# Kernel optimization log

Measured on AMD Instinct MI355X. Metric: run time of the kernel, lower is better.

The kernel has to match this reference:

```python
import jax, jax.numpy as jnp
import numpy as np

N = 50000
IN_F = 128
OUT_F = 128
NRELA = 128
E1 = 400000
E2 = 100000
ALPHA = 0.2   # LeakyReLU slope
D = 0.85      # PageRank damping
EPS = 1e-12


def setup_inputs() -> dict:
    key = jax.random.key(0)
    ks = jax.random.split(key, 8)
    return {
        "input": jax.random.normal(ks[0], (N, IN_F), dtype=jnp.float32),
        "edge": jax.random.randint(ks[1], (2, E1), 0, N, dtype=jnp.int64),
        "edge_embed": jax.random.normal(ks[2], (E1, NRELA), dtype=jnp.float32),
        "edge_list_nhop": jax.random.randint(ks[3], (2, E2), 0, N, dtype=jnp.int64),
        "edge_embed_nhop": jax.random.normal(ks[4], (E2, NRELA), dtype=jnp.float32),
        "entity_rank": jax.random.uniform(ks[5], (N,), dtype=jnp.float32),
        "a": 0.05 * jax.random.normal(ks[6], (OUT_F, 2 * IN_F + NRELA), dtype=jnp.float32),
        "a_2": 0.05 * jax.random.normal(ks[7], (1, OUT_F), dtype=jnp.float32),
    }


def reference(input, edge, edge_embed, edge_list_nhop, edge_embed_nhop, entity_rank, a, a_2):
    n = input.shape[0]
    # concat n-hop edges (len(edge_list_nhop) != 0 path in the original)
    e = jnp.concatenate([edge, edge_list_nhop], axis=1)          # [2, E]
    emb = jnp.concatenate([edge_embed, edge_embed_nhop], axis=0) # [E, nrela]
    src, dst = e[0], e[1]

    # edge MLP: edge_h = [x_src | x_dst | rel]  -> a @ edge_h^T, leakyrelu
    edge_h = jnp.concatenate([input[src], input[dst], emb], axis=1)   # [E, 2*in+nrela]
    edge_m = jax.nn.leaky_relu(edge_h @ a.T, ALPHA)                   # [E, out]
    powers = -jax.nn.leaky_relu(edge_m @ a_2[0], ALPHA)               # [E]
    edge_e = jnp.exp(powers)                                          # [E]

    # softmax-like normalization over incoming edges of each target node
    a_rowsum = jax.ops.segment_sum(edge_e, dst, num_segments=n)       # [N]
    a_rowsum = jnp.where(a_rowsum == 0.0, EPS, a_rowsum)
    rel_att = edge_e / a_rowsum[dst]                                  # [E]

    # PageRank-style rank update
    e_rowsum = jax.ops.segment_sum(rel_att, src, num_segments=n)      # [N] (out-sum)
    e_rowsum = jnp.where(e_rowsum == 0.0, EPS, e_rowsum)
    val = rel_att * entity_rank[src] / e_rowsum[src]                  # [E]
    e_colsum = jax.ops.segment_sum(val, dst, num_segments=n)          # [N]
    new_rank = 1.0 - D + D * e_colsum                                 # [N]

    # rank-weighted attention propagation of edge features
    edge_prop = (rel_att * new_rank[src])[:, None] * edge_m           # [E, out]
    h_prime = jax.ops.segment_sum(edge_prop, dst, num_segments=n)     # [N, out]

    return jax.nn.elu(h_prime), new_rank
```

## Files before the change

kernel.cpp:

```cpp
#include <hip/hip_runtime.h>
#include <math.h>

#define N_NODES 50000
#define E1N 400000
#define E2N 100000
#define E_TOT 500000
#define ALPHAC 0.2f
#define DAMP 0.85f
#define EPSC 1e-12f

typedef __bf16 bf16_t;
typedef __bf16 bf16x4 __attribute__((ext_vector_type(4)));
typedef __bf16 bf16x8 __attribute__((ext_vector_type(8)));
typedef _Float16 f16_t;
typedef _Float16 f16x4 __attribute__((ext_vector_type(4)));
typedef float f32x4 __attribute__((ext_vector_type(4)));
typedef float f32x16 __attribute__((ext_vector_type(16)));

__device__ __forceinline__ float lrelu(float x) { return x > 0.f ? x : ALPHAC * x; }

__global__ __launch_bounds__(256) void k_pack12(const float* __restrict__ a,
                                                bf16_t* __restrict__ bp) {
  int i = blockIdx.x * 256 + threadIdx.x;
  if (i >= 32768) return;
  int j = i & 7;
  int l = (i >> 3) & 63;
  int nt = (i >> 9) & 7;
  int ks = i >> 12;
  int c = nt * 32 + (l & 31);
  int o = (c < 128) ? c : c - 128;
  int koff = (c < 128) ? 0 : 128;
  int k = ks * 16 + ((l >> 5) << 3) + j;
  bp[i] = (bf16_t)a[o * 384 + koff + k];
}

__global__ __launch_bounds__(256) void k_pack3(const float* __restrict__ a,
                                               bf16_t* __restrict__ bp) {
  int i = blockIdx.x * 256 + threadIdx.x;
  if (i >= 16384) return;
  int j = i & 7;
  int l = (i >> 3) & 63;
  int nt = (i >> 9) & 3;
  int ks = i >> 11;
  int o = nt * 32 + (l & 31);
  int k = ks * 16 + ((l >> 5) << 3) + j;
  bp[i] = (bf16_t)a[o * 384 + 256 + k];
}

__global__ __launch_bounds__(256) void k_pack3c(const float* __restrict__ a,
                                                bf16_t* __restrict__ bp) {
  int i = blockIdx.x * 256 + threadIdx.x;
  if (i >= 16384) return;
  int j = i & 7;
  int l = (i >> 3) & 63;
  int nt = (i >> 9) & 7;
  int ks = i >> 12;
  int o = nt * 16 + (l & 15);
  int k = ks * 32 + ((l >> 4) << 3) + j;
  bp[i] = (bf16_t)a[o * 384 + 256 + k];
}

__global__ __launch_bounds__(256) void k_cnt(const int* __restrict__ edge,
                                             const int* __restrict__ nhop,
                                             int stride, int* __restrict__ cnt) {
  int e = blockIdx.x * 256 + threadIdx.x;
  if (e >= E_TOT) return;
  int d = (e < E1N) ? edge[(size_t)(E1N + e) * stride]
                    : nhop[(size_t)(E2N + (e - E1N)) * stride];
  atomicAdd(&cnt[d], 1);
}

__global__ __launch_bounds__(256) void k_edges(const int* __restrict__ edge,
                                               const int* __restrict__ nhop,
                                               int* __restrict__ sidx,
                                               int* __restrict__ didx, int stride) {
  int e = blockIdx.x * 256 + threadIdx.x;
  if (e >= E_TOT) return;
  int s, d;
  if (e < E1N) {
    s = edge[(size_t)e * stride];
    d = edge[(size_t)(E1N + e) * stride];
  } else {
    int t = e - E1N;
    s = nhop[(size_t)t * stride];
    d = nhop[(size_t)(E2N + t) * stride];
  }
  sidx[e] = s;
  didx[e] = d;
}

__global__ __launch_bounds__(256) void k_scan(const int* __restrict__ cnt,
                                              int* __restrict__ csr_start,
                                              int* __restrict__ cursor) {
  __shared__ int ls[256];
  __shared__ int lofs[256];
  int t = threadIdx.x;
  int lo = t * 196, hi = lo + 196;
  if (hi > N_NODES) hi = N_NODES;
  int s = 0;
  for (int i = lo; i < hi; ++i) s += cnt[i];
  ls[t] = s;
  __syncthreads();
  if (t == 0) {
    int run = 0;
    for (int i = 0; i < 256; ++i) { lofs[i] = run; run += ls[i]; }
  }
  __syncthreads();
  int run = lofs[t];
  for (int i = lo; i < hi; ++i) {
    csr_start[i] = run;
    cursor[i] = run;
    run += cnt[i];
  }
}

__global__ __launch_bounds__(256) void k_pos2(const int* __restrict__ edge,
                                              const int* __restrict__ nhop,
                                              int stride, int* __restrict__ cursor,
                                              int* __restrict__ epos,
                                              int* __restrict__ sidx_s,
                                              int* __restrict__ didx_s) {
  int e = blockIdx.x * 256 + threadIdx.x;
  if (e >= E_TOT) return;
  int s, d;
  if (e < E1N) {
    s = edge[(size_t)e * stride];
    d = edge[(size_t)(E1N + e) * stride];
  } else {
    int t = e - E1N;
    s = nhop[(size_t)t * stride];
    d = nhop[(size_t)(E2N + t) * stride];
  }
  int pos = atomicAdd(&cursor[d], 1);
  epos[e] = pos;
  sidx_s[pos] = s;
  didx_s[pos] = d;
}

__global__ __launch_bounds__(256) void k_uv2(const float* __restrict__ input,
                                             const bf16_t* __restrict__ bp12,
                                             bf16_t* __restrict__ uv) {
  const int tid = threadIdx.x, lane = tid & 63, wv = tid >> 6;
  const int blk = blockIdx.x >> 1, half = blockIdx.x & 1;
  const int ntoff = half * 4;
  const int n0 = blk * 128 + wv * 32;
  const int m = lane & 31, hi2 = lane >> 5;
  int n = n0 + m;
  if (n >= N_NODES) n = 0;
  const float* ar = input + (size_t)n * 128 + hi2 * 8;
  const bf16x8* bp = (const bf16x8*)bp12;

  f32x16 acc[4];
#pragma unroll
  for (int nt = 0; nt < 4; ++nt)
#pragma unroll
    for (int r = 0; r < 16; ++r) acc[nt][r] = 0.f;

#pragma unroll
  for (int ks = 0; ks < 8; ++ks) {
    float4 u0 = *(const float4*)(ar + ks * 16);
    float4 u1 = *(const float4*)(ar + ks * 16 + 4);
    bf16x8 af = {(bf16_t)u0.x, (bf16_t)u0.y, (bf16_t)u0.z, (bf16_t)u0.w,
                 (bf16_t)u1.x, (bf16_t)u1.y, (bf16_t)u1.z, (bf16_t)u1.w};
#pragma unroll
    for (int nt = 0; nt < 4; ++nt)
      acc[nt] = __builtin_amdgcn_mfma_f32_32x32x16_bf16(
          af, bp[(ks * 8 + ntoff + nt) * 64 + lane], acc[nt], 0, 0, 0);
  }
#pragma unroll
  for (int nt = 0; nt < 4; ++nt)
#pragma unroll
    for (int r = 0; r < 16; ++r) {
      int row = (r & 3) + ((r >> 2) << 3) + (hi2 << 2);
      int node = n0 + row;
      if (node < N_NODES)
        uv[(size_t)node * 256 + (ntoff + nt) * 32 + m] = (bf16_t)acc[nt][r];
    }
}

__global__ __launch_bounds__(256) void k_passA4(
    const float* __restrict__ eemb, const float* __restrict__ eembn,
    const bf16_t* __restrict__ uv, const int* __restrict__ edge,
    const int* __restrict__ nhop, int stride, const int* __restrict__ epos,
    const bf16_t* __restrict__ bp3c, const float* __restrict__ a2,
    float* __restrict__ edge_e_s, float* __restrict__ a_rowsum,
    bf16_t* __restrict__ P) {
  __shared__ __align__(16) char sA[16384];
  __shared__ __align__(16) char sB[32768];
  const int tid = threadIdx.x;
  const long long e0 = (long long)blockIdx.x * 64;
  const int lane = tid & 63;

  const int strow = tid >> 5;
  const int stcol = (tid & 31) * 4;
  float4 rg[8];
#pragma unroll
  for (int s = 0; s < 8; ++s) {
    int row = s * 8 + strow;
    long long e = e0 + row;
    rg[s] = make_float4(0.f, 0.f, 0.f, 0.f);
    if (e < E_TOT) {
      const float* src = (e < E1N) ? eemb + (size_t)e * 128
                                   : eembn + (size_t)(e - E1N) * 128;
      rg[s] = *(const float4*)(src + stcol);
    }
  }
  int4 rb[8];
  {
    const int4* bsrc = (const int4*)bp3c;
#pragma unroll
    for (int i = 0; i < 8; ++i) rb[i] = bsrc[i * 256 + tid];
  }
  const int g = tid >> 5;
  const int ml = tid & 31;
  int sarr[8], darr[8], parr[8];
#pragma unroll
  for (int i = 0; i < 8; ++i) {
    long long e = e0 + i * 8 + g;
    sarr[i] = 0; darr[i] = 0; parr[i] = 0;
    if (e < E_TOT) {
      if (e < E1N) {
        sarr[i] = edge[(size_t)e * stride];
        darr[i] = edge[(size_t)(E1N + e) * stride];
      } else {
        long long t = e - E1N;
        sarr[i] = nhop[(size_t)t * stride];
        darr[i] = nhop[(size_t)(E2N + t) * stride];
      }
      parr[i] = epos[e];
    }
  }
#pragma unroll
  for (int s = 0; s < 8; ++s) {
    int row = s * 8 + strow;
    bf16x4 b = {(bf16_t)rg[s].x, (bf16_t)rg[s].y, (bf16_t)rg[s].z, (bf16_t)rg[s].w};
    *(bf16x4*)(sA + row * 256 + ((stcol * 2) ^ ((row & 7) << 4))) = b;
  }
  {
    int4* bdst = (int4*)sB;
#pragma unroll
    for (int i = 0; i < 8; ++i) bdst[i * 256 + tid] = rb[i];
  }
  const int cl = ml * 4;
  bf16x4 uu[8], vv[8];
#pragma unroll
  for (int i = 0; i < 8; ++i) {
    uu[i] = *(const bf16x4*)(uv + (size_t)sarr[i] * 256 + cl);
    vv[i] = *(const bf16x4*)(uv + (size_t)darr[i] * 256 + 128 + cl);
  }
  __syncthreads();

  const int wv = tid >> 6;
  const int cc = lane & 15, kg = lane >> 4;
  const int arow = wv * 16 + cc;
  const int swz = (arow & 7) << 4;
  const bf16x8* sBv = (const bf16x8*)sB;

  f32x4 acc[8];
#pragma unroll
  for (int nt = 0; nt < 8; ++nt) acc[nt] = (f32x4){0.f, 0.f, 0.f, 0.f};

#pragma unroll
  for (int ks = 0; ks < 4; ++ks) {
    bf16x8 af = *(const bf16x8*)(sA + arow * 256 + ((ks * 64 + kg * 16) ^ swz));
#pragma unroll
    for (int nt = 0; nt < 8; ++nt)
      acc[nt] = __builtin_amdgcn_mfma_f32_16x16x32_bf16(
          af, sBv[(ks * 8 + nt) * 64 + lane], acc[nt], 0, 0, 0);
  }
  __syncthreads();

#pragma unroll
  for (int nt = 0; nt < 8; ++nt)
#pragma unroll
    for (int r = 0; r < 4; ++r) {
      int row = wv * 16 + kg * 4 + r;
      int cb = (nt * 16 + cc) * 2;
      *(f16_t*)(sA + row * 256 + (cb ^ ((row & 7) << 4))) = (f16_t)acc[nt][r];
    }
  __syncthreads();

  {
    const float4 a2v = *(const float4*)(a2 + cl);
#pragma unroll
    for (int i = 0; i < 8; ++i) {
      int row = i * 8 + g;
      long long e = e0 + row;
      if (e < E_TOT) {
        f16x4 cc4 = *(const f16x4*)(sA + row * 256 + ((cl * 2) ^ ((row & 7) << 4)));
        float p0 = lrelu((float)cc4[0] + (float)uu[i][0] + (float)vv[i][0]);
        float p1 = lrelu((float)cc4[1] + (float)uu[i][1] + (float)vv[i][1]);
        float p2 = lrelu((float)cc4[2] + (float)uu[i][2] + (float)vv[i][2]);
        float p3 = lrelu((float)cc4[3] + (float)uu[i][3] + (float)vv[i][3]);
        bf16x4 po = {(bf16_t)p0, (bf16_t)p1, (bf16_t)p2, (bf16_t)p3};
        *(bf16x4*)(P + (size_t)parr[i] * 128 + cl) = po;
        float sac = p0 * a2v.x + p1 * a2v.y + p2 * a2v.z + p3 * a2v.w;
#pragma unroll
        for (int off = 1; off < 32; off <<= 1) sac += __shfl_xor(sac, off, 64);
        if (ml == 0) {
          float ev = expf(-lrelu(sac));
          edge_e_s[parr[i]] = ev;
          atomicAdd(&a_rowsum[darr[i]], ev);
        }
      }
    }
  }
}

__global__ __launch_bounds__(256) void k_hprime_s(
    const bf16_t* __restrict__ P, const int* __restrict__ csr_start,
    const int* __restrict__ cnt, const float* __restrict__ rel_att_s,
    const int* __restrict__ sidx_s, const float* __restrict__ new_rank,
    float* __restrict__ out) {
  int gnode = (blockIdx.x << 3) | (threadIdx.x >> 5);
  if (gnode >= N_NODES) return;
  int m = threadIdx.x & 31;
  int start = csr_start[gnode], deg = cnt[gnode];
  float a0 = 0.f, a1 = 0.f, a2v = 0.f, a3v = 0.f;
  if (deg > 0) {
    float rel_c = rel_att_s[start];
    float rk_c = new_rank[sidx_s[start]];
    bf16x4 p_c = *(const bf16x4*)(P + (size_t)start * 128 + m * 4);
    for (int i = 0; i < deg; ++i) {
      int qn = start + ((i + 1 < deg) ? i + 1 : i);
      float rel_n = rel_att_s[qn];
      float rk_n = new_rank[sidx_s[qn]];
      bf16x4 p_n = *(const bf16x4*)(P + (size_t)qn * 128 + m * 4);
      float we = rel_c * rk_c;
      a0 += we * (float)p_c[0];
      a1 += we * (float)p_c[1];
      a2v += we * (float)p_c[2];
      a3v += we * (float)p_c[3];
      rel_c = rel_n; rk_c = rk_n; p_c = p_n;
    }
  }
  float4 r;
  r.x = a0 > 0.f ? a0 : expm1f(a0);
  r.y = a1 > 0.f ? a1 : expm1f(a1);
  r.z = a2v > 0.f ? a2v : expm1f(a2v);
  r.w = a3v > 0.f ? a3v : expm1f(a3v);
  *(float4*)(out + (size_t)gnode * 128 + m * 4) = r;
}

template <bool ACCUM>
__global__ __launch_bounds__(256, 3) void k_pass(
    const float* __restrict__ eemb, const float* __restrict__ eembn,
    const bf16_t* __restrict__ uv, const int* __restrict__ sidx,
    const int* __restrict__ didx, const bf16_t* __restrict__ bp3,
    const float* __restrict__ a2, float* __restrict__ edge_e,
    float* __restrict__ a_rowsum, const float* __restrict__ rel_att,
    const float* __restrict__ new_rank, float* __restrict__ hout) {
  __shared__ bf16_t s_sum[128][136];
  const int tid = threadIdx.x;
  const long long e0 = (long long)blockIdx.x * 128;
  {
    const int g = tid >> 5;
    const int cl = (tid & 31) * 4;
#pragma unroll
    for (int i = 0; i < 16; ++i) {
      int el = i * 8 + g;
      long long e = e0 + el;
      float sx = 0.f, sy = 0.f, sz = 0.f, sw = 0.f;
      if (e < E_TOT) {
        int s = sidx[e], d = didx[e];
        bf16x4 u = *(const bf16x4*)(uv + (size_t)s * 256 + cl);
        bf16x4 v = *(const bf16x4*)(uv + (size_t)d * 256 + 128 + cl);
        sx = (float)u[0] + (float)v[0];
        sy = (float)u[1] + (float)v[1];
        sz = (float)u[2] + (float)v[2];
        sw = (float)u[3] + (float)v[3];
      }
      bf16x4 o = {(bf16_t)sx, (bf16_t)sy, (bf16_t)sz, (bf16_t)sw};
      *(bf16x4*)&s_sum[el][cl] = o;
    }
  }
  __syncthreads();

  const int lane = tid & 63;
  const int wv = tid >> 6;
  const long long e0w = e0 + wv * 32;
  if (e0w >= E_TOT) return;
  const int m = lane & 31, hi2 = lane >> 5;
  const long long e = e0w + m;
  const float* b2 = (e < E1N) ? (eemb + (size_t)e * 128)
                              : (eembn + (size_t)(e - E1N) * 128);
  const float* ar = b2 + hi2 * 8;

  const bf16x8* bp = (const bf16x8*)bp3;
  f32x16 acc[4];
#pragma unroll
  for (int nt = 0; nt < 4; ++nt)
#pragma unroll
    for (int r = 0; r < 16; ++r) acc[nt][r] = 0.f;

  auto loadA = [&](int ks) -> bf16x8 {
    float4 u0 = *(const float4*)(ar + ks * 16);
    float4 u1 = *(const float4*)(ar + ks * 16 + 4);
    bf16x8 rr = {(bf16_t)u0.x, (bf16_t)u0.y, (bf16_t)u0.z, (bf16_t)u0.w,
                 (bf16_t)u1.x, (bf16_t)u1.y, (bf16_t)u1.z, (bf16_t)u1.w};
    return rr;
  };

  bf16x8 a_cur = loadA(0);
  bf16x8 bb[4], bn[4];
#pragma unroll
  for (int nt = 0; nt < 4; ++nt) bb[nt] = bp[nt * 64 + lane];

#pragma unroll
  for (int ks = 0; ks < 8; ++ks) {
    bf16x8 a_nxt;
    if (ks < 7) {
      a_nxt = loadA(ks + 1);
#pragma unroll
      for (int nt = 0; nt < 4; ++nt) bn[nt] = bp[((ks + 1) * 4 + nt) * 64 + lane];
    }
#pragma unroll
    for (int nt = 0; nt < 4; ++nt)
      acc[nt] = __builtin_amdgcn_mfma_f32_32x32x16_bf16(a_cur, bb[nt], acc[nt], 0, 0, 0);
    a_cur = a_nxt;
#pragma unroll
    for (int nt = 0; nt < 4; ++nt) bb[nt] = bn[nt];
  }

  if (!ACCUM) {
    float sac[16];
#pragma unroll
    for (int r = 0; r < 16; ++r) sac[r] = 0.f;
#pragma unroll
    for (int nt = 0; nt < 4; ++nt) {
      float a2v = a2[nt * 32 + m];
      int o = nt * 32 + m;
#pragma unroll
      for (int r = 0; r < 16; ++r) {
        int row = (r & 3) + ((r >> 2) << 3) + (hi2 << 2);
        float c = acc[nt][r] + (float)s_sum[wv * 32 + row][o];
        sac[r] += lrelu(c) * a2v;
      }
    }
#pragma unroll
    for (int off = 1; off < 32; off <<= 1) {
#pragma unroll
      for (int r = 0; r < 16; ++r) sac[r] += __shfl_xor(sac[r], off, 64);
    }
    if (m == 0) {
#pragma unroll
      for (int r = 0; r < 16; ++r) {
        int row = (r & 3) + ((r >> 2) << 3) + (hi2 << 2);
        long long ee_i = e0w + row;
        float ev = expf(-lrelu(sac[r]));
        edge_e[ee_i] = ev;
        atomicAdd(&a_rowsum[didx[ee_i]], ev);
      }
    }
  } else {
    float w_m = rel_att[e] * new_rank[sidx[e]];
    int d = didx[e];
    float wr[16];
    int dr[16];
#pragma unroll
    for (int r = 0; r < 16; ++r) {
      int row = (r & 3) + ((r >> 2) << 3) + (hi2 << 2);
      wr[r] = __shfl(w_m, row, 64);
      dr[r] = __shfl(d, row, 64);
    }
#pragma unroll
    for (int nt = 0; nt < 4; ++nt) {
      int o = nt * 32 + m;
#pragma unroll
      for (int r = 0; r < 16; ++r) {
        int row = (r & 3) + ((r >> 2) << 3) + (hi2 << 2);
        float c = acc[nt][r] + (float)s_sum[wv * 32 + row][o];
        atomicAdd(&hout[(size_t)dr[r] * 128 + o], lrelu(c) * wr[r]);
      }
    }
  }
}

__global__ __launch_bounds__(256) void k_relatt(const float* __restrict__ edge_e,
                                                const int* __restrict__ didx,
                                                const int* __restrict__ sidx,
                                                const float* __restrict__ a_rowsum,
                                                float* __restrict__ rel_att,
                                                float* __restrict__ e_rowsum) {
  int e = blockIdx.x * 256 + threadIdx.x;
  if (e >= E_TOT) return;
  float rs = a_rowsum[didx[e]];
  rs = (rs == 0.f) ? EPSC : rs;
  float r = edge_e[e] / rs;
  rel_att[e] = r;
  atomicAdd(&e_rowsum[sidx[e]], r);
}

__global__ __launch_bounds__(256) void k_val(const float* __restrict__ rel_att,
                                             const int* __restrict__ sidx,
                                             const int* __restrict__ didx,
                                             const float* __restrict__ rank,
                                             const float* __restrict__ e_rowsum,
                                             float* __restrict__ e_colsum) {
  int e = blockIdx.x * 256 + threadIdx.x;
  if (e >= E_TOT) return;
  int s = sidx[e];
  float er = e_rowsum[s];
  er = (er == 0.f) ? EPSC : er;
  float val = rel_att[e] * rank[s] / er;
  atomicAdd(&e_colsum[didx[e]], val);
}

__global__ __launch_bounds__(256) void k_rank(const float* __restrict__ e_colsum,
                                              float* __restrict__ new_rank,
                                              float* __restrict__ out_tail) {
  int n = blockIdx.x * 256 + threadIdx.x;
  if (n >= N_NODES) return;
  float nr = 1.f - DAMP + DAMP * e_colsum[n];
  new_rank[n] = nr;
  out_tail[n] = nr;
}

__global__ __launch_bounds__(256) void k_elu(float* __restrict__ h) {
  int i = blockIdx.x * 256 + threadIdx.x;
  if (i < N_NODES * 128) {
    float x = h[i];
    h[i] = x > 0.f ? x : expm1f(x);
  }
}

extern "C" void kernel_launch(void* const* d_in, const int* in_sizes, int n_in,
                              void* d_out, int out_size, void* d_ws, size_t ws_size,
                              hipStream_t stream) {
  const float* input = (const float*)d_in[0];
  const int* edge = (const int*)d_in[1];
  const float* eemb = (const float*)d_in[2];
  const int* enh = (const int*)d_in[3];
  const float* eembn = (const float*)d_in[4];
  const float* rank = (const float*)d_in[5];
  const float* a = (const float*)d_in[6];
  const float* a2 = (const float*)d_in[7];
  float* out = (float*)d_out;

  int estride = (in_sizes[1] == 2 * E1N) ? 1 : 2;

  char* ws = (char*)d_ws;
  bf16_t* bp12 = (bf16_t*)(ws);
  bf16_t* bp3s = (bf16_t*)(ws + 65536);
  bf16_t* uv = (bf16_t*)(ws + 98304);
  int* epos = (int*)(ws + 25698304);
  int* sidx_s = (int*)(ws + 27698304);
  int* didx_s = (int*)(ws + 29698304);
  float* edge_e_s = (float*)(ws + 31698304);
  int* csr_start = (int*)(ws + 33698304);
  int* cursor = (int*)(ws + 33898304);
  int* cnt = (int*)(ws + 34098304);
  float* a_rowsum = (float*)(ws + 34298304);
  float* e_rowsum = (float*)(ws + 34498304);
  float* e_colsum = (float*)(ws + 34698304);
  float* new_rank = (float*)(ws + 34898304);
  bf16_t* P = (bf16_t*)(ws + 35098624);

  const bool big = ws_size >= 163098624ULL;

  const int NB = (E_TOT + 127) / 128;
  const int NB4 = (E_TOT + 63) / 64;
  const int EB = (E_TOT + 255) / 256;
  const int UVB = 2 * ((N_NODES + 127) / 128);

  if (big) {
    hipMemsetAsync(cnt, 0, 4 * 200000, stream);

    k_pack12<<<128, 256, 0, stream>>>(a, bp12);
    k_pack3c<<<64, 256, 0, stream>>>(a, bp3s);
    k_cnt<<<EB, 256, 0, stream>>>(edge, enh, estride, cnt);
    k_scan<<<1, 256, 0, stream>>>(cnt, csr_start, cursor);
    k_pos2<<<EB, 256, 0, stream>>>(edge, enh, estride, cursor, epos, sidx_s, didx_s);
    k_uv2<<<UVB, 256, 0, stream>>>(input, bp12, uv);

    k_passA4<<<NB4, 256, 0, stream>>>(eemb, eembn, uv, edge, enh, estride, epos,
                                      bp3s, a2, edge_e_s, a_rowsum, P);
    k_relatt<<<EB, 256, 0, stream>>>(edge_e_s, didx_s, sidx_s, a_rowsum,
                                     edge_e_s, e_rowsum);
    k_val<<<EB, 256, 0, stream>>>(edge_e_s, sidx_s, didx_s, rank, e_rowsum, e_colsum);
    k_rank<<<(N_NODES + 255) / 256, 256, 0, stream>>>(e_colsum, new_rank,
                                                      out + (size_t)N_NODES * 128);
    k_hprime_s<<<(N_NODES + 7) / 8, 256, 0, stream>>>(P, csr_start, cnt, edge_e_s,
                                                      sidx_s, new_rank, out);
  } else {
    int* sidx_fb = epos;
    int* didx_fb = sidx_s;
    float* rel_fb = (float*)didx_s;
    float* ee_fb = edge_e_s;

    hipMemsetAsync(cnt, 0, 4 * 200000, stream);
    hipMemsetAsync(out, 0, (size_t)N_NODES * 128 * 4, stream);

    k_pack12<<<128, 256, 0, stream>>>(a, bp12);
    k_pack3<<<64, 256, 0, stream>>>(a, bp3s);
    k_edges<<<EB, 256, 0, stream>>>(edge, enh, sidx_fb, didx_fb, estride);
    k_uv2<<<UVB, 256, 0, stream>>>(input, bp12, uv);

    k_pass<false><<<NB, 256, 0, stream>>>(eemb, eembn, uv, sidx_fb, didx_fb, bp3s,
                                          a2, ee_fb, a_rowsum, nullptr, nullptr,
                                          nullptr);
    k_relatt<<<EB, 256, 0, stream>>>(ee_fb, didx_fb, sidx_fb, a_rowsum, rel_fb,
                                     e_rowsum);
    k_val<<<EB, 256, 0, stream>>>(rel_fb, sidx_fb, didx_fb, rank, e_rowsum, e_colsum);
    k_rank<<<(N_NODES + 255) / 256, 256, 0, stream>>>(e_colsum, new_rank,
                                                      out + (size_t)N_NODES * 128);
    k_pass<true><<<NB, 256, 0, stream>>>(eemb, eembn, uv, sidx_fb, didx_fb, bp3s,
                                         a2, nullptr, nullptr, rel_fb, new_rank, out);
    k_elu<<<(N_NODES * 128 + 255) / 256, 256, 0, stream>>>(out);
  }
}
```

Baseline: 753.4 us.

## Rewrite node projection with 16x16 MFMA tiles and read edge-pass weights from global

```diff
diff --git a/kernel.cpp b/kernel.cpp
--- a/kernel.cpp
+++ b/kernel.cpp
@@ -31,6 +31,21 @@
   int o = (c < 128) ? c : c - 128;
   int koff = (c < 128) ? 0 : 128;
   int k = ks * 16 + ((l >> 5) << 3) + j;
+  bp[i] = (bf16_t)a[o * 384 + koff + k];
+}
+
+__global__ __launch_bounds__(256) void k_pack12c(const float* __restrict__ a,
+                                                 bf16_t* __restrict__ bp) {
+  int i = blockIdx.x * 256 + threadIdx.x;
+  if (i >= 32768) return;
+  int j = i & 7;
+  int l = (i >> 3) & 63;
+  int nt = (i >> 9) & 15;
+  int ks = i >> 13;
+  int c = nt * 16 + (l & 15);
+  int o = (c < 128) ? c : c - 128;
+  int koff = (c < 128) ? 0 : 128;
+  int k = ks * 32 + ((l >> 4) << 3) + j;
   bp[i] = (bf16_t)a[o * 384 + koff + k];
 }
 
@@ -178,7 +193,72 @@
     }
 }
 
-__global__ __launch_bounds__(256) void k_passA4(
+__global__ __launch_bounds__(256) void k_uv3(const float* __restrict__ input,
+                                             const bf16_t* __restrict__ bp12c,
+                                             bf16_t* __restrict__ uv) {
+  __shared__ __align__(16) char sA[16384];
+  const int tid = threadIdx.x;
+  const int n0 = blockIdx.x * 64;
+
+#pragma unroll
+  for (int s = 0; s < 8; ++s) {
+    int idx = s * 1024 + tid * 4;
+    int row = idx >> 7, col = idx & 127;
+    int n = n0 + row;
+    float4 u = make_float4(0.f, 0.f, 0.f, 0.f);
+    if (n < N_NODES) u = *(const float4*)(input + (size_t)n * 128 + col);
+    bf16x4 b = {(bf16_t)u.x, (bf16_t)u.y, (bf16_t)u.z, (bf16_t)u.w};
+    *(bf16x4*)(sA + row * 256 + ((col * 2) ^ ((row & 7) << 4))) = b;
+  }
+  __syncthreads();
+
+  const int lane = tid & 63, wv = tid >> 6;
+  const int cc = lane & 15, kg = lane >> 4;
+  const int arow = wv * 16 + cc;
+  const int swz = (arow & 7) << 4;
+  const bf16x8* bp = (const bf16x8*)bp12c;
+
+  f32x4 acc[16];
+#pragma unroll
+  for (int nt = 0; nt < 16; ++nt) acc[nt] = (f32x4){0.f, 0.f, 0.f, 0.f};
+
+#pragma unroll
+  for (int ks = 0; ks < 4; ++ks) {
+    bf16x8 af = *(const bf16x8*)(sA + arow * 256 + ((ks * 64 + kg * 16) ^ swz));
+#pragma unroll
+    for (int nt = 0; nt < 16; ++nt)
+      acc[nt] = __builtin_amdgcn_mfma_f32_16x16x32_bf16(
+          af, bp[(ks * 16 + nt) * 64 + lane], acc[nt], 0, 0, 0);
+  }
+
+#pragma unroll
+  for (int h = 0; h < 2; ++h) {
+    __syncthreads();
+#pragma unroll
+    for (int nt = 0; nt < 8; ++nt)
+#pragma unroll
+      for (int r = 0; r < 4; ++r) {
+        int row = wv * 16 + kg * 4 + r;
+        int cb = (nt * 16 + cc) * 2;
+        *(bf16_t*)(sA + row * 256 + (cb ^ ((row & 7) << 4))) =
+            (bf16_t)acc[h * 8 + nt][r];
+      }
+    __syncthreads();
+    const int rr = tid >> 4;
+    const int cb2 = (tid & 15) * 16;
+#pragma unroll
+    for (int i = 0; i < 4; ++i) {
+      int row = i * 16 + rr;
+      int n = n0 + row;
+      if (n < N_NODES) {
+        bf16x8 v = *(const bf16x8*)(sA + row * 256 + (cb2 ^ ((row & 7) << 4)));
+        *(bf16x8*)(uv + (size_t)n * 256 + h * 128 + (cb2 >> 1)) = v;
+      }
+    }
+  }
+}
+
+__global__ __launch_bounds__(256) void k_passA5(
     const float* __restrict__ eemb, const float* __restrict__ eembn,
     const bf16_t* __restrict__ uv, const int* __restrict__ edge,
     const int* __restrict__ nhop, int stride, const int* __restrict__ epos,
@@ -186,33 +266,27 @@
     float* __restrict__ edge_e_s, float* __restrict__ a_rowsum,
     bf16_t* __restrict__ P) {
   __shared__ __align__(16) char sA[16384];
-  __shared__ __align__(16) char sB[32768];
   const int tid = threadIdx.x;
   const long long e0 = (long long)blockIdx.x * 64;
-  const int lane = tid & 63;
-
-  const int strow = tid >> 5;
-  const int stcol = (tid & 31) * 4;
-  float4 rg[8];
+
 #pragma unroll
   for (int s = 0; s < 8; ++s) {
-    int row = s * 8 + strow;
+    int idx = s * 1024 + tid * 4;
+    int row = idx >> 7, col = idx & 127;
     long long e = e0 + row;
-    rg[s] = make_float4(0.f, 0.f, 0.f, 0.f);
+    float4 u = make_float4(0.f, 0.f, 0.f, 0.f);
     if (e < E_TOT) {
       const float* src = (e < E1N) ? eemb + (size_t)e * 128
                                    : eembn + (size_t)(e - E1N) * 128;
-      rg[s] = *(const float4*)(src + stcol);
-    }
-  }
-  int4 rb[8];
-  {
-    const int4* bsrc = (const int4*)bp3c;
-#pragma unroll
-    for (int i = 0; i < 8; ++i) rb[i] = bsrc[i * 256 + tid];
-  }
+      u = *(const float4*)(src + col);
+    }
+    bf16x4 b = {(bf16_t)u.x, (bf16_t)u.y, (bf16_t)u.z, (bf16_t)u.w};
+    *(bf16x4*)(sA + row * 256 + ((col * 2) ^ ((row & 7) << 4))) = b;
+  }
+
   const int g = tid >> 5;
   const int ml = tid & 31;
+  const int cl = ml * 4;
   int sarr[8], darr[8], parr[8];
 #pragma unroll
   for (int i = 0; i < 8; ++i) {
@@ -230,31 +304,20 @@
       parr[i] = epos[e];
     }
   }
-#pragma unroll
-  for (int s = 0; s < 8; ++s) {
-    int row = s * 8 + strow;
-    bf16x4 b = {(bf16_t)rg[s].x, (bf16_t)rg[s].y, (bf16_t)rg[s].z, (bf16_t)rg[s].w};
-    *(bf16x4*)(sA + row * 256 + ((stcol * 2) ^ ((row & 7) << 4))) = b;
-  }
-  {
-    int4* bdst = (int4*)sB;
-#pragma unroll
-    for (int i = 0; i < 8; ++i) bdst[i * 256 + tid] = rb[i];
-  }
-  const int cl = ml * 4;
+  __syncthreads();
+
   bf16x4 uu[8], vv[8];
 #pragma unroll
   for (int i = 0; i < 8; ++i) {
     uu[i] = *(const bf16x4*)(uv + (size_t)sarr[i] * 256 + cl);
     vv[i] = *(const bf16x4*)(uv + (size_t)darr[i] * 256 + 128 + cl);
   }
-  __syncthreads();
-
-  const int wv = tid >> 6;
+
+  const int lane = tid & 63, wv = tid >> 6;
   const int cc = lane & 15, kg = lane >> 4;
   const int arow = wv * 16 + cc;
   const int swz = (arow & 7) << 4;
-  const bf16x8* sBv = (const bf16x8*)sB;
+  const bf16x8* bp = (const bf16x8*)bp3c;
 
   f32x4 acc[8];
 #pragma unroll
@@ -266,7 +329,7 @@
 #pragma unroll
     for (int nt = 0; nt < 8; ++nt)
       acc[nt] = __builtin_amdgcn_mfma_f32_16x16x32_bf16(
-          af, sBv[(ks * 8 + nt) * 64 + lane], acc[nt], 0, 0, 0);
+          af, bp[(ks * 8 + nt) * 64 + lane], acc[nt], 0, 0, 0);
   }
   __syncthreads();
 
@@ -559,21 +622,22 @@
   const bool big = ws_size >= 163098624ULL;
 
   const int NB = (E_TOT + 127) / 128;
-  const int NB4 = (E_TOT + 63) / 64;
+  const int NB5 = (E_TOT + 63) / 64;
   const int EB = (E_TOT + 255) / 256;
-  const int UVB = 2 * ((N_NODES + 127) / 128);
+  const int UVB2 = 2 * ((N_NODES + 127) / 128);
+  const int UVB3 = (N_NODES + 63) / 64;
 
   if (big) {
     hipMemsetAsync(cnt, 0, 4 * 200000, stream);
 
-    k_pack12<<<128, 256, 0, stream>>>(a, bp12);
+    k_pack12c<<<128, 256, 0, stream>>>(a, bp12);
     k_pack3c<<<64, 256, 0, stream>>>(a, bp3s);
     k_cnt<<<EB, 256, 0, stream>>>(edge, enh, estride, cnt);
     k_scan<<<1, 256, 0, stream>>>(cnt, csr_start, cursor);
     k_pos2<<<EB, 256, 0, stream>>>(edge, enh, estride, cursor, epos, sidx_s, didx_s);
-    k_uv2<<<UVB, 256, 0, stream>>>(input, bp12, uv);
-
-    k_passA4<<<NB4, 256, 0, stream>>>(eemb, eembn, uv, edge, enh, estride, epos,
+    k_uv3<<<UVB3, 256, 0, stream>>>(input, bp12, uv);
+
+    k_passA5<<<NB5, 256, 0, stream>>>(eemb, eembn, uv, edge, enh, estride, epos,
                                       bp3s, a2, edge_e_s, a_rowsum, P);
     k_relatt<<<EB, 256, 0, stream>>>(edge_e_s, didx_s, sidx_s, a_rowsum,
                                      edge_e_s, e_rowsum);
@@ -594,7 +658,7 @@
     k_pack12<<<128, 256, 0, stream>>>(a, bp12);
     k_pack3<<<64, 256, 0, stream>>>(a, bp3s);
     k_edges<<<EB, 256, 0, stream>>>(edge, enh, sidx_fb, didx_fb, estride);
-    k_uv2<<<UVB, 256, 0, stream>>>(input, bp12, uv);
+    k_uv2<<<UVB2, 256, 0, stream>>>(input, bp12, uv);
 
     k_pass<false><<<NB, 256, 0, stream>>>(eemb, eembn, uv, sidx_fb, didx_fb, bp3s,
                                           a2, ee_fb, a_rowsum, nullptr, nullptr,
```

Result: no change. 765.0 us (+1.5%).
